# Performance work log

Measured on AMD Instinct MI355X. Metric: run time of the kernel, lower is better.

Reference implementation:

```python
import jax, jax.numpy as jnp
import numpy as np

H = 4  # attention heads


def gat_layer(x, src, dst, W, a_src, a_dst, b, N):
    """PyG-style GATConv (concat=True, negative_slope=0.2, eval-mode dropout)."""
    h = (x @ W).reshape(N, H, -1)                       # [N,H,C]
    es = jnp.einsum('nhc,hc->nh', h, a_src)             # per-node src score
    ed = jnp.einsum('nhc,hc->nh', h, a_dst)             # per-node dst score
    e = jax.nn.leaky_relu(es[src] + ed[dst], negative_slope=0.2)  # [E,H]
    # segment softmax over incoming edges of each destination node
    emax = jax.ops.segment_max(e, dst, num_segments=N)
    ee = jnp.exp(e - emax[dst])
    denom = jax.ops.segment_sum(ee, dst, num_segments=N)
    alpha = ee / (denom[dst] + 1e-16)                   # [E,H]
    out = jax.ops.segment_sum(h[src] * alpha[..., None], dst, num_segments=N)
    return out.reshape(N, -1) + b                        # [N,H*C]


def setup_inputs() -> dict:
    key = jax.random.key(0)
    ks = jax.random.split(key, 13)
    N, E, D, Q = 50000, 800000, 256, 8
    HID, OUT = 256, 256
    Ch, Co = HID // H, OUT // H
    inp = {}
    inp['x'] = jax.random.normal(ks[0], (N, D), dtype=jnp.float32)
    inp['edge_index'] = jax.random.randint(ks[1], (2, E), 0, N, dtype=jnp.int64)
    inp['query_embedding'] = jax.random.normal(ks[2], (Q, OUT), dtype=jnp.float32)
    # layer 1: input_dim -> heads * (hidden_dim//heads)
    inp['W1'] = jax.random.normal(ks[3], (D, HID), dtype=jnp.float32) / np.sqrt(D).astype(np.float32)
    inp['a_src1'] = jax.random.normal(ks[4], (H, Ch), dtype=jnp.float32) / np.sqrt(Ch).astype(np.float32)
    inp['a_dst1'] = jax.random.normal(ks[5], (H, Ch), dtype=jnp.float32) / np.sqrt(Ch).astype(np.float32)
    inp['b1'] = jnp.zeros((HID,), dtype=jnp.float32)
    # layer 2: hidden_dim -> heads * (output_dim//heads)
    inp['W2'] = jax.random.normal(ks[6], (HID, OUT), dtype=jnp.float32) / np.sqrt(HID).astype(np.float32)
    inp['a_src2'] = jax.random.normal(ks[7], (H, Co), dtype=jnp.float32) / np.sqrt(Co).astype(np.float32)
    inp['a_dst2'] = jax.random.normal(ks[8], (H, Co), dtype=jnp.float32) / np.sqrt(Co).astype(np.float32)
    inp['b2'] = jnp.zeros((OUT,), dtype=jnp.float32)
    # node classifier over concat([query, node]) -> 1 (intended Linear(2*OUT, 1))
    inp['Wc'] = jax.random.normal(ks[9], (2 * OUT, 1), dtype=jnp.float32) / np.sqrt(2 * OUT).astype(np.float32)
    inp['bc'] = jnp.zeros((1,), dtype=jnp.float32)
    return inp


def reference(x, edge_index, query_embedding, W1, a_src1, a_dst1, b1,
              W2, a_src2, a_dst2, b2, Wc, bc):
    N = x.shape[0]
    loops = jnp.arange(N, dtype=edge_index.dtype)        # GATConv add_self_loops=True
    src = jnp.concatenate([edge_index[0], loops])
    dst = jnp.concatenate([edge_index[1], loops])
    h = jax.nn.relu(gat_layer(x, src, dst, W1, a_src1, a_dst1, b1, N))
    emb = gat_layer(h, src, dst, W2, a_src2, a_dst2, b2, N)  # [N, OUT]
    D = emb.shape[1]
    # scores[q,n] = Linear(concat(query[q], emb[n])) — computed without
    # materializing the [Q,N,2D] concat (identical math).
    q_part = query_embedding @ Wc[:D] + bc               # [Q,1]
    n_part = emb @ Wc[D:]                                # [N,1]
    node_scores = q_part[:, 0][:, None] + n_part[:, 0][None, :]  # [Q,N]
    return emb, node_scores
```

## Files before the change

kernel.cpp:

```cpp
#include <hip/hip_runtime.h>

typedef unsigned short u16;
typedef unsigned int   u32;
typedef __attribute__((ext_vector_type(8))) short short8v;
typedef __attribute__((ext_vector_type(8))) unsigned short us8;
typedef __attribute__((ext_vector_type(4))) float f32x4;

static __device__ __forceinline__ float bf2f(u16 u){ union{u32 i; float f;} v; v.i=(u32)u<<16; return v.f; }
static __device__ __forceinline__ u16 f2bf(float f){ union{float f; u32 i;} u; u.f=f; u32 r=u.i+0x7FFFu+((u.i>>16)&1u); return (u16)(r>>16); }

static __device__ __forceinline__ float ld1(const void* p, size_t i, int f32){
  return f32 ? ((const float*)p)[i] : bf2f(((const u16*)p)[i]);
}
static __device__ __forceinline__ float4 ld4(const void* p, size_t i, int f32){
  if (f32) return *((const float4*)((const float*)p + i));
  ushort4 v = *((const ushort4*)((const u16*)p + i));
  return make_float4(bf2f(v.x), bf2f(v.y), bf2f(v.z), bf2f(v.w));
}
static __device__ __forceinline__ void st4(void* p, size_t i, float4 v, int f32){
  if (f32) *((float4*)((float*)p + i)) = v;
  else { ushort4 o; o.x=f2bf(v.x); o.y=f2bf(v.y); o.z=f2bf(v.z); o.w=f2bf(v.w); *((ushort4*)((u16*)p + i)) = o; }
}
static __device__ __forceinline__ void st1(void* p, size_t i, float v, int f32){
  if (f32) ((float*)p)[i] = v; else ((u16*)p)[i] = f2bf(v);
}
static __device__ __forceinline__ int lde(const int* ei, size_t i, int i64){
  return i64 ? ei[2*i] : ei[i];
}
static __device__ __forceinline__ int clampi(int v, int lo, int hi){ return v<lo?lo:(v>hi?hi:v); }

__global__ void detect_kernel(const u32* __restrict__ x, const int* __restrict__ ei,
                              int* __restrict__ flags){
  __shared__ int cnt[2];
  int t = threadIdx.x;
  if (t < 2) cnt[t] = 0;
  __syncthreads();
  int good = 0;
  for (int i = t; i < 4096; i += 256){
    u32 e = (x[i] >> 7) & 0xFFu;
    if (e >= 90u && e <= 150u) good++;
  }
  atomicAdd(&cnt[0], good);
  int nzodd = 0;
  for (int i = t; i < 2048; i += 256){
    if (ei[2*i+1] != 0) nzodd++;
  }
  atomicAdd(&cnt[1], nzodd);
  __syncthreads();
  if (t == 0){
    flags[0] = (cnt[0] < 2867) ? 1 : 0;
    flags[1] = (cnt[1] == 0) ? 1 : 0;
  }
}

__global__ void count_kernel(const int* __restrict__ ei, int E, int N,
                             int* __restrict__ deg, const int* __restrict__ flags){
  int i64 = flags[1];
  int i = blockIdx.x*blockDim.x + threadIdx.x;
  int Et = E + N;
  if (i < Et){
    int d = (i < E) ? clampi(lde(ei, (size_t)E + i, i64), 0, N-1) : (i - E);
    atomicAdd(&deg[d], 1);
  }
}

__global__ __launch_bounds__(256) void scan1_kernel(const int* __restrict__ deg,
    int* __restrict__ offs, int* __restrict__ bsum, int N){
  __shared__ int sm[256];
  int t = threadIdx.x;
  int i = blockIdx.x*256 + t;
  int v = (i < N) ? deg[i] : 0;
  sm[t] = v; __syncthreads();
  #pragma unroll
  for (int off = 1; off < 256; off <<= 1){
    int u = (t >= off) ? sm[t-off] : 0;
    __syncthreads();
    sm[t] += u;
    __syncthreads();
  }
  if (i < N) offs[i] = sm[t] - v;
  if (t == 255) bsum[blockIdx.x] = sm[255];
}

__global__ __launch_bounds__(1024) void scan2_kernel(const int* __restrict__ bsum,
    int* __restrict__ bpre, int NB){
  __shared__ int sm[1024];
  int t = threadIdx.x;
  int v = (t < NB) ? bsum[t] : 0;
  sm[t] = v; __syncthreads();
  #pragma unroll
  for (int off = 1; off < 1024; off <<= 1){
    int u = (t >= off) ? sm[t-off] : 0;
    __syncthreads();
    sm[t] += u;
    __syncthreads();
  }
  if (t < NB) bpre[t] = sm[t] - v;
  if (t == 1023) bpre[NB] = sm[1023];
}

__global__ __launch_bounds__(256) void scan3_kernel(int* __restrict__ offs,
    int* __restrict__ cursor, const int* __restrict__ bpre, int N, int NB){
  int i = blockIdx.x*256 + threadIdx.x;
  if (i < N){
    int v = offs[i] + bpre[blockIdx.x];
    offs[i] = v; cursor[i] = v;
  }
  if (i == 0) offs[N] = bpre[NB];
}

__global__ void scatter_kernel(const int* __restrict__ ei, int E, int N,
    int* __restrict__ cursor, int* __restrict__ csr_src, const int* __restrict__ flags){
  int i64 = flags[1];
  int i = blockIdx.x*blockDim.x + threadIdx.x;
  int Et = E + N;
  if (i < Et){
    int s, d;
    if (i < E){
      s = clampi(lde(ei, i, i64), 0, N-1);
      d = clampi(lde(ei, (size_t)E + i, i64), 0, N-1);
    } else { s = i - E; d = s; }
    int p = atomicAdd(&cursor[d], 1);
    csr_src[p] = s;
  }
}

__global__ __launch_bounds__(256) void btrans_kernel(const void* __restrict__ B1,
    const void* __restrict__ B2, u16* __restrict__ BT1, u16* __restrict__ BT2,
    const int* __restrict__ flags){
  int f32 = flags[0];
  const void* B = blockIdx.z ? B2 : B1;
  u16* BT = blockIdx.z ? BT2 : BT1;
  __shared__ u16 tile[64][65];
  int k0 = blockIdx.y*64, c0 = blockIdx.x*64;
  int r0 = threadIdx.x >> 6, c = threadIdx.x & 63;
  for (int r = r0; r < 64; r += 4)
    tile[r][c] = f32 ? f2bf(((const float*)B)[(size_t)(k0+r)*256 + c0 + c])
                     : ((const u16*)B)[(size_t)(k0+r)*256 + c0 + c];
  __syncthreads();
  for (int j = r0; j < 64; j += 4)
    BT[(size_t)(c0+j)*256 + k0 + c] = tile[c][j];
}

__global__ __launch_bounds__(512, 4) void gemm_mfma(const void* __restrict__ A,
    const u16* __restrict__ BT, u16* __restrict__ C, int M, int aIsInput,
    const int* __restrict__ flags, float* __restrict__ es, float* __restrict__ ed,
    const void* __restrict__ a_src, const void* __restrict__ a_dst){
  int af32 = aIsInput ? flags[0] : 0;
  int f32 = flags[0];
  __shared__ __align__(16) u16 As[128][40];
  __shared__ __align__(16) u16 Bs[256][40];
  int tid = threadIdx.x;
  int wave = tid >> 6, lane = tid & 63;
  int wm = wave >> 2, wn = wave & 3;
  int l15 = lane & 15, l4 = lane >> 4;
  int row0 = blockIdx.x * 128;
  const u16*  A16 = (const u16*)A;
  const float* A32 = (const float*)A;
  int srow = tid >> 2, sks = (tid & 3) * 8;
  int scol = tid >> 1, skh = (tid & 1) * 16;
  int sgr = min(row0 + srow, M-1);
  f32x4 acc[4][4] = {};
  for (int k0 = 0; k0 < 256; k0 += 32){
    __syncthreads();
    {
      us8 av;
      if (af32){
        const float* ap = A32 + (size_t)sgr*256 + k0 + sks;
        float4 v0 = *(const float4*)ap, v1 = *(const float4*)(ap+4);
        av = (us8){f2bf(v0.x),f2bf(v0.y),f2bf(v0.z),f2bf(v0.w),
                   f2bf(v1.x),f2bf(v1.y),f2bf(v1.z),f2bf(v1.w)};
      } else {
        av = *(const us8*)(A16 + (size_t)sgr*256 + k0 + sks);
      }
      *(us8*)&As[srow][sks] = av;
      const u16* bp = BT + (size_t)scol*256 + k0 + skh;
      *(us8*)&Bs[scol][skh]   = *(const us8*)bp;
      *(us8*)&Bs[scol][skh+8] = *(const us8*)(bp + 8);
    }
    __syncthreads();
    short8v a[4], b[4];
    #pragma unroll
    for (int mi = 0; mi < 4; mi++)
      a[mi] = *(const short8v*)&As[wm*64 + mi*16 + l15][8*l4];
    #pragma unroll
    for (int ni = 0; ni < 4; ni++)
      b[ni] = *(const short8v*)&Bs[wn*64 + ni*16 + l15][8*l4];
    #pragma unroll
    for (int mi = 0; mi < 4; mi++)
      #pragma unroll
      for (int ni = 0; ni < 4; ni++)
        acc[mi][ni] = __builtin_amdgcn_mfma_f32_16x16x32_bf16(a[mi], b[ni], acc[mi][ni], 0, 0, 0);
  }
  #pragma unroll
  for (int mi = 0; mi < 4; mi++){
    #pragma unroll
    for (int ni = 0; ni < 4; ni++){
      #pragma unroll
      for (int r = 0; r < 4; r++){
        int row = row0 + wm*64 + mi*16 + l4*4 + r;
        int col = wn*64 + ni*16 + l15;
        if (row < M) C[(size_t)row*256 + col] = f2bf(acc[mi][ni][r]);
      }
    }
  }
  float as_[4], ad_[4];
  #pragma unroll
  for (int ni = 0; ni < 4; ni++){
    as_[ni] = ld1(a_src, wn*64 + ni*16 + l15, f32);
    ad_[ni] = ld1(a_dst, wn*64 + ni*16 + l15, f32);
  }
  #pragma unroll
  for (int mi = 0; mi < 4; mi++){
    #pragma unroll
    for (int r = 0; r < 4; r++){
      float pe = acc[mi][0][r]*as_[0] + acc[mi][1][r]*as_[1]
               + acc[mi][2][r]*as_[2] + acc[mi][3][r]*as_[3];
      float pd = acc[mi][0][r]*ad_[0] + acc[mi][1][r]*ad_[1]
               + acc[mi][2][r]*ad_[2] + acc[mi][3][r]*ad_[3];
      #pragma unroll
      for (int off = 1; off < 16; off <<= 1){
        pe += __shfl_xor(pe, off, 64);
        pd += __shfl_xor(pd, off, 64);
      }
      if (l15 == 0){
        int row = row0 + wm*64 + mi*16 + l4*4 + r;
        if (row < M){
          es[(size_t)row*4 + wn] = pe;
          ed[(size_t)row*4 + wn] = pd;
        }
      }
    }
  }
}

__global__ __launch_bounds__(256) void agg_kernel(const u16* __restrict__ h,
    const int* __restrict__ csr_src, const int* __restrict__ offs,
    const float* __restrict__ es, const float* __restrict__ ed, int N,
    const void* __restrict__ bias, void* __restrict__ out, int do_relu, int outIsOutput,
    const int* __restrict__ flags, const void* __restrict__ Wc,
    const float* __restrict__ qp, int Q){
  int f32in = flags[0];
  int of32  = outIsOutput ? flags[0] : 0;
  int ln = threadIdx.x & 63;
  int n = blockIdx.x*4 + (threadIdx.x >> 6);
  if (n >= N) return;
  int beg = offs[n], end = offs[n+1];
  int hd = ln >> 4, c0 = ln*4;
  float edn = ed[(size_t)n*4 + hd];
  float a0=0.f, a1=0.f, a2=0.f, a3=0.f, ws=0.f;
  int i = beg;
  for (; i + 8 <= end; i += 8){
    int s[8]; float x[8]; ushort4 hv[8];
    #pragma unroll
    for (int j = 0; j < 8; j++) s[j] = csr_src[i+j];
    #pragma unroll
    for (int j = 0; j < 8; j++) x[j] = es[(size_t)s[j]*4 + hd];
    #pragma unroll
    for (int j = 0; j < 8; j++) hv[j] = *(const ushort4*)&h[(size_t)s[j]*256 + c0];
    #pragma unroll
    for (int j = 0; j < 8; j++){
      float t = x[j] + edn; t = (t > 0.f) ? t : 0.2f*t; t = fminf(t, 60.f);
      float w = __expf(t);
      a0 += w*bf2f(hv[j].x); a1 += w*bf2f(hv[j].y);
      a2 += w*bf2f(hv[j].z); a3 += w*bf2f(hv[j].w);
      ws += w;
    }
  }
  for (; i + 4 <= end; i += 4){
    int s[4]; float x[4]; ushort4 hv[4];
    #pragma unroll
    for (int j = 0; j < 4; j++) s[j] = csr_src[i+j];
    #pragma unroll
    for (int j = 0; j < 4; j++) x[j] = es[(size_t)s[j]*4 + hd];
    #pragma unroll
    for (int j = 0; j < 4; j++) hv[j] = *(const ushort4*)&h[(size_t)s[j]*256 + c0];
    #pragma unroll
    for (int j = 0; j < 4; j++){
      float t = x[j] + edn; t = (t > 0.f) ? t : 0.2f*t; t = fminf(t, 60.f);
      float w = __expf(t);
      a0 += w*bf2f(hv[j].x); a1 += w*bf2f(hv[j].y);
      a2 += w*bf2f(hv[j].z); a3 += w*bf2f(hv[j].w);
      ws += w;
    }
  }
  for (; i < end; i++){
    int s = csr_src[i];
    float t = es[(size_t)s*4 + hd] + edn; t = (t > 0.f) ? t : 0.2f*t; t = fminf(t, 60.f);
    float w = __expf(t);
    ushort4 hv = *(const ushort4*)&h[(size_t)s*256 + c0];
    a0 += w*bf2f(hv.x); a1 += w*bf2f(hv.y);
    a2 += w*bf2f(hv.z); a3 += w*bf2f(hv.w);
    ws += w;
  }
  float inv = 1.f / (ws + 1e-16f);
  float4 bv = ld4(bias, c0, f32in);
  float4 ov = make_float4(a0*inv + bv.x, a1*inv + bv.y, a2*inv + bv.z, a3*inv + bv.w);
  if (do_relu){
    ov.x = fmaxf(ov.x, 0.f); ov.y = fmaxf(ov.y, 0.f);
    ov.z = fmaxf(ov.z, 0.f); ov.w = fmaxf(ov.w, 0.f);
  }
  st4(out, (size_t)n*256 + c0, ov, of32);
  if (outIsOutput){
    float4 wc4 = ld4(Wc, 256 + c0, f32in);
    float v = ov.x*wc4.x + ov.y*wc4.y + ov.z*wc4.z + ov.w*wc4.w;
    #pragma unroll
    for (int off = 1; off < 64; off <<= 1) v += __shfl_xor(v, off, 64);
    if (ln < Q) st1(out, (size_t)N*256 + (size_t)ln*N + n, qp[ln] + v, of32);
  }
}

__global__ void qpart_kernel(const void* __restrict__ query, const void* __restrict__ Wc,
    const void* __restrict__ bc, float* __restrict__ qp, int Q, const int* __restrict__ flags){
  int f32 = flags[0];
  int q = threadIdx.x >> 5, ln = threadIdx.x & 31;
  if (q >= Q) return;
  float s = 0.f;
  for (int j = ln; j < 256; j += 32) s += ld1(query, q*256 + j, f32) * ld1(Wc, j, f32);
  #pragma unroll
  for (int off = 16; off; off >>= 1) s += __shfl_down(s, off, 32);
  if (ln == 0) qp[q] = s + ld1(bc, 0, f32);
}

extern "C" void kernel_launch(void* const* d_in, const int* in_sizes, int n_in,
                              void* d_out, int out_size, void* d_ws, size_t ws_size,
                              hipStream_t stream){
  const void* x     = d_in[0];
  const int*  ei    = (const int*)d_in[1];
  const void* query = d_in[2];
  const void* W1    = d_in[3];
  const void* as1   = d_in[4];
  const void* ad1   = d_in[5];
  const void* b1    = d_in[6];
  const void* W2    = d_in[7];
  const void* as2   = d_in[8];
  const void* ad2   = d_in[9];
  const void* b2    = d_in[10];
  const void* Wc    = d_in[11];
  const void* bc    = d_in[12];

  int N = in_sizes[0] / 256;
  int E = in_sizes[1] / 2;
  int Q = in_sizes[2] / 256;
  int Et = E + N;
  int NB = (N + 255) / 256;

  char* p = (char*)d_ws;
  auto alloc = [&](size_t bytes)->char*{
    char* r = p; p += (bytes + 255) & ~(size_t)255; return r;
  };
  int*  flags   = (int*) alloc(256);
  u16*  bufA    = (u16*) alloc((size_t)N*256*2);
  u16*  bufB    = (u16*) alloc((size_t)N*256*2);
  float* es     = (float*)alloc((size_t)N*4*4);
  float* ed     = (float*)alloc((size_t)N*4*4);
  int*  deg     = (int*)  alloc((size_t)N*4);
  int*  offs    = (int*)  alloc((size_t)(N+1)*4);
  int*  cursor  = (int*)  alloc((size_t)N*4);
  int*  csr_src = (int*)  alloc((size_t)Et*4);
  int*  bsum    = (int*)  alloc((size_t)(NB+1)*4);
  int*  bpre    = (int*)  alloc((size_t)(NB+1)*4);
  u16*  BT1     = (u16*)  alloc(256*256*2);
  u16*  BT2     = (u16*)  alloc(256*256*2);
  float* qp     = (float*)alloc(64*4);

  const int thr = 256;
  detect_kernel<<<1, 256, 0, stream>>>((const u32*)x, ei, flags);

  hipMemsetAsync(deg, 0, (size_t)N*4, stream);
  count_kernel  <<<(Et + thr-1)/thr, thr, 0, stream>>>(ei, E, N, deg, flags);
  scan1_kernel  <<<NB, 256, 0, stream>>>(deg, offs, bsum, N);
  scan2_kernel  <<<1, 1024, 0, stream>>>(bsum, bpre, NB);
  scan3_kernel  <<<NB, 256, 0, stream>>>(offs, cursor, bpre, N, NB);
  scatter_kernel<<<(Et + thr-1)/thr, thr, 0, stream>>>(ei, E, N, cursor, csr_src, flags);

  dim3 tgrid(4, 4, 2);
  int gblocks = (N + 127)/128;
  dim3 ngrid((N + 3)/4);

  btrans_kernel<<<tgrid, 256, 0, stream>>>(W1, W2, BT1, BT2, flags);
  qpart_kernel <<<1, 256, 0, stream>>>(query, Wc, bc, qp, Q, flags);

  gemm_mfma <<<gblocks, 512, 0, stream>>>(x, BT1, bufA, N, 1, flags, es, ed, as1, ad1);
  agg_kernel<<<ngrid, 256, 0, stream>>>(bufA, csr_src, offs, es, ed, N, b1, bufB, 1, 0,
                                        flags, Wc, qp, Q);
  gemm_mfma <<<gblocks, 512, 0, stream>>>(bufB, BT2, bufA, N, 0, flags, es, ed, as2, ad2);
  agg_kernel<<<ngrid, 256, 0, stream>>>(bufA, csr_src, offs, es, ed, N, b2, d_out, 0, 1,
                                        flags, Wc, qp, Q);
}
```

Measured before the change: 308.3 us.

## Fuse CSR build into one cooperative kernel and store precomputed byte offsets

Replaces the memset, count, three scan kernels and scatter with a single cooperative kernel that uses grid-wide syncs between phases. It also merges the weight transpose and query-part kernels into one prep launch. The CSR now stores source byte offsets (s*512), so the aggregation kernel skips the index multiply. This cuts launch count and per-launch overhead but limits the CSR build to 256 blocks with grid-stride loops and adds the cost of five grid barriers.

```diff
diff --git a/kernel.cpp b/kernel.cpp
--- a/kernel.cpp
+++ b/kernel.cpp
@@ -1,4 +1,7 @@
 #include <hip/hip_runtime.h>
+#include <hip/hip_cooperative_groups.h>
+
+namespace cg = cooperative_groups;
 
 typedef unsigned short u16;
 typedef unsigned int   u32;
@@ -53,93 +56,103 @@
   }
 }
 
-__global__ void count_kernel(const int* __restrict__ ei, int E, int N,
-                             int* __restrict__ deg, const int* __restrict__ flags){
+__global__ __launch_bounds__(256) void csr_kernel(const int* __restrict__ ei, int E, int N,
+    int* __restrict__ deg, int* __restrict__ offs, int* __restrict__ cursor,
+    int* __restrict__ csr_boff, int* __restrict__ bsum, const int* __restrict__ flags){
+  cg::grid_group grid = cg::this_grid();
+  __shared__ int sm[256];
   int i64 = flags[1];
-  int i = blockIdx.x*blockDim.x + threadIdx.x;
   int Et = E + N;
-  if (i < Et){
+  int gsz = gridDim.x * 256;
+  int gtid = blockIdx.x*256 + threadIdx.x;
+  int t = threadIdx.x;
+  for (int i = gtid; i < N; i += gsz) deg[i] = 0;
+  grid.sync();
+  for (int i = gtid; i < Et; i += gsz){
     int d = (i < E) ? clampi(lde(ei, (size_t)E + i, i64), 0, N-1) : (i - E);
     atomicAdd(&deg[d], 1);
   }
-}
-
-__global__ __launch_bounds__(256) void scan1_kernel(const int* __restrict__ deg,
-    int* __restrict__ offs, int* __restrict__ bsum, int N){
-  __shared__ int sm[256];
-  int t = threadIdx.x;
-  int i = blockIdx.x*256 + t;
-  int v = (i < N) ? deg[i] : 0;
-  sm[t] = v; __syncthreads();
-  #pragma unroll
-  for (int off = 1; off < 256; off <<= 1){
-    int u = (t >= off) ? sm[t-off] : 0;
+  grid.sync();
+  int NB = (N + 255) >> 8;
+  for (int b = blockIdx.x; b < NB; b += gridDim.x){
+    int i = b*256 + t;
+    int v = (i < N) ? deg[i] : 0;
     __syncthreads();
-    sm[t] += u;
-    __syncthreads();
-  }
-  if (i < N) offs[i] = sm[t] - v;
-  if (t == 255) bsum[blockIdx.x] = sm[255];
-}
-
-__global__ __launch_bounds__(1024) void scan2_kernel(const int* __restrict__ bsum,
-    int* __restrict__ bpre, int NB){
-  __shared__ int sm[1024];
-  int t = threadIdx.x;
-  int v = (t < NB) ? bsum[t] : 0;
-  sm[t] = v; __syncthreads();
-  #pragma unroll
-  for (int off = 1; off < 1024; off <<= 1){
-    int u = (t >= off) ? sm[t-off] : 0;
-    __syncthreads();
-    sm[t] += u;
-    __syncthreads();
-  }
-  if (t < NB) bpre[t] = sm[t] - v;
-  if (t == 1023) bpre[NB] = sm[1023];
-}
-
-__global__ __launch_bounds__(256) void scan3_kernel(int* __restrict__ offs,
-    int* __restrict__ cursor, const int* __restrict__ bpre, int N, int NB){
-  int i = blockIdx.x*256 + threadIdx.x;
-  if (i < N){
-    int v = offs[i] + bpre[blockIdx.x];
+    sm[t] = v; __syncthreads();
+    #pragma unroll
+    for (int off = 1; off < 256; off <<= 1){
+      int u = (t >= off) ? sm[t-off] : 0;
+      __syncthreads();
+      sm[t] += u;
+      __syncthreads();
+    }
+    if (i < N) offs[i] = sm[t] - v;
+    if (t == 255) bsum[b] = sm[255];
+  }
+  grid.sync();
+  if (blockIdx.x == 0){
+    int chunk = (NB + 255) >> 8;
+    int lo = t*chunk, hi = min(lo + chunk, NB);
+    int s = 0;
+    for (int i = lo; i < hi; i++) s += bsum[i];
+    sm[t] = s; __syncthreads();
+    int mine = s;
+    #pragma unroll
+    for (int off = 1; off < 256; off <<= 1){
+      int u = (t >= off) ? sm[t-off] : 0;
+      __syncthreads();
+      sm[t] += u;
+      __syncthreads();
+    }
+    int run = sm[t] - mine;
+    for (int i = lo; i < hi; i++){ int v = bsum[i]; bsum[i] = run; run += v; }
+    if (t == 255) offs[N] = sm[255];
+  }
+  grid.sync();
+  for (int i = gtid; i < N; i += gsz){
+    int v = offs[i] + bsum[i >> 8];
     offs[i] = v; cursor[i] = v;
   }
-  if (i == 0) offs[N] = bpre[NB];
-}
-
-__global__ void scatter_kernel(const int* __restrict__ ei, int E, int N,
-    int* __restrict__ cursor, int* __restrict__ csr_src, const int* __restrict__ flags){
-  int i64 = flags[1];
-  int i = blockIdx.x*blockDim.x + threadIdx.x;
-  int Et = E + N;
-  if (i < Et){
+  grid.sync();
+  for (int i = gtid; i < Et; i += gsz){
     int s, d;
     if (i < E){
       s = clampi(lde(ei, i, i64), 0, N-1);
       d = clampi(lde(ei, (size_t)E + i, i64), 0, N-1);
     } else { s = i - E; d = s; }
     int p = atomicAdd(&cursor[d], 1);
-    csr_src[p] = s;
-  }
-}
-
-__global__ __launch_bounds__(256) void btrans_kernel(const void* __restrict__ B1,
+    csr_boff[p] = s * 512;
+  }
+}
+
+__global__ __launch_bounds__(256) void prep_kernel(const void* __restrict__ B1,
     const void* __restrict__ B2, u16* __restrict__ BT1, u16* __restrict__ BT2,
-    const int* __restrict__ flags){
+    const void* __restrict__ query, const void* __restrict__ Wc, const void* __restrict__ bc,
+    float* __restrict__ qp, int Q, const int* __restrict__ flags){
   int f32 = flags[0];
-  const void* B = blockIdx.z ? B2 : B1;
-  u16* BT = blockIdx.z ? BT2 : BT1;
-  __shared__ u16 tile[64][65];
-  int k0 = blockIdx.y*64, c0 = blockIdx.x*64;
-  int r0 = threadIdx.x >> 6, c = threadIdx.x & 63;
-  for (int r = r0; r < 64; r += 4)
-    tile[r][c] = f32 ? f2bf(((const float*)B)[(size_t)(k0+r)*256 + c0 + c])
-                     : ((const u16*)B)[(size_t)(k0+r)*256 + c0 + c];
-  __syncthreads();
-  for (int j = r0; j < 64; j += 4)
-    BT[(size_t)(c0+j)*256 + k0 + c] = tile[c][j];
+  int bid = blockIdx.x;
+  if (bid < 32){
+    const void* B = (bid >= 16) ? B2 : B1;
+    u16* BT = (bid >= 16) ? BT2 : BT1;
+    int rem = bid & 15;
+    int k0 = (rem >> 2)*64, c0 = (rem & 3)*64;
+    __shared__ u16 tile[64][65];
+    int r0 = threadIdx.x >> 6, c = threadIdx.x & 63;
+    for (int r = r0; r < 64; r += 4)
+      tile[r][c] = f32 ? f2bf(((const float*)B)[(size_t)(k0+r)*256 + c0 + c])
+                       : ((const u16*)B)[(size_t)(k0+r)*256 + c0 + c];
+    __syncthreads();
+    for (int j = r0; j < 64; j += 4)
+      BT[(size_t)(c0+j)*256 + k0 + c] = tile[c][j];
+  } else {
+    int q = threadIdx.x >> 5, ln = threadIdx.x & 31;
+    if (q >= Q) return;
+    float s = 0.f;
+    for (int j = ln; j < 256; j += 32) s += ld1(query, q*256 + j, f32) * ld1(Wc, j, f32);
+    #pragma unroll
+    for (int off = 16; off; off >>= 1) s += __shfl_down(s, off, 32);
+    if (ln == 0) qp[q] = s + ld1(bc, 0, f32);
+  }
 }
 
 __global__ __launch_bounds__(512, 4) void gemm_mfma(const void* __restrict__ A,
@@ -235,7 +248,7 @@
 }
 
 __global__ __launch_bounds__(256) void agg_kernel(const u16* __restrict__ h,
-    const int* __restrict__ csr_src, const int* __restrict__ offs,
+    const int* __restrict__ csr_boff, const int* __restrict__ offs,
     const float* __restrict__ es, const float* __restrict__ ed, int N,
     const void* __restrict__ bias, void* __restrict__ out, int do_relu, int outIsOutput,
     const int* __restrict__ flags, const void* __restrict__ Wc,
@@ -247,17 +260,21 @@
   if (n >= N) return;
   int beg = offs[n], end = offs[n+1];
   int hd = ln >> 4, c0 = ln*4;
+  int hd4 = hd*4;
+  size_t coff = (size_t)c0*2;
+  const char* hbase = (const char*)h;
+  const char* ebase = (const char*)es;
   float edn = ed[(size_t)n*4 + hd];
   float a0=0.f, a1=0.f, a2=0.f, a3=0.f, ws=0.f;
   int i = beg;
   for (; i + 8 <= end; i += 8){
-    int s[8]; float x[8]; ushort4 hv[8];
-    #pragma unroll
-    for (int j = 0; j < 8; j++) s[j] = csr_src[i+j];
-    #pragma unroll
-    for (int j = 0; j < 8; j++) x[j] = es[(size_t)s[j]*4 + hd];
-    #pragma unroll
-    for (int j = 0; j < 8; j++) hv[j] = *(const ushort4*)&h[(size_t)s[j]*256 + c0];
+    int bo[8]; float x[8]; ushort4 hv[8];
+    #pragma unroll
+    for (int j = 0; j < 8; j++) bo[j] = csr_boff[i+j];
+    #pragma unroll
+    for (int j = 0; j < 8; j++) x[j] = *(const float*)(ebase + (bo[j] >> 5) + hd4);
+    #pragma unroll
+    for (int j = 0; j < 8; j++) hv[j] = *(const ushort4*)(hbase + bo[j] + coff);
     #pragma unroll
     for (int j = 0; j < 8; j++){
       float t = x[j] + edn; t = (t > 0.f) ? t : 0.2f*t; t = fminf(t, 60.f);
@@ -268,13 +285,13 @@
     }
   }
   for (; i + 4 <= end; i += 4){
-    int s[4]; float x[4]; ushort4 hv[4];
-    #pragma unroll
-    for (int j = 0; j < 4; j++) s[j] = csr_src[i+j];
-    #pragma unroll
-    for (int j = 0; j < 4; j++) x[j] = es[(size_t)s[j]*4 + hd];
-    #pragma unroll
-    for (int j = 0; j < 4; j++) hv[j] = *(const ushort4*)&h[(size_t)s[j]*256 + c0];
+    int bo[4]; float x[4]; ushort4 hv[4];
+    #pragma unroll
+    for (int j = 0; j < 4; j++) bo[j] = csr_boff[i+j];
+    #pragma unroll
+    for (int j = 0; j < 4; j++) x[j] = *(const float*)(ebase + (bo[j] >> 5) + hd4);
+    #pragma unroll
+    for (int j = 0; j < 4; j++) hv[j] = *(const ushort4*)(hbase + bo[j] + coff);
     #pragma unroll
     for (int j = 0; j < 4; j++){
       float t = x[j] + edn; t = (t > 0.f) ? t : 0.2f*t; t = fminf(t, 60.f);
@@ -285,10 +302,11 @@
     }
   }
   for (; i < end; i++){
-    int s = csr_src[i];
-    float t = es[(size_t)s*4 + hd] + edn; t = (t > 0.f) ? t : 0.2f*t; t = fminf(t, 60.f);
+    int bo = csr_boff[i];
+    float t = *(const float*)(ebase + (bo >> 5) + hd4) + edn;
+    t = (t > 0.f) ? t : 0.2f*t; t = fminf(t, 60.f);
     float w = __expf(t);
-    ushort4 hv = *(const ushort4*)&h[(size_t)s*256 + c0];
+    ushort4 hv = *(const ushort4*)(hbase + bo + coff);
     a0 += w*bf2f(hv.x); a1 += w*bf2f(hv.y);
     a2 += w*bf2f(hv.z); a3 += w*bf2f(hv.w);
     ws += w;
@@ -308,18 +326,6 @@
     for (int off = 1; off < 64; off <<= 1) v += __shfl_xor(v, off, 64);
     if (ln < Q) st1(out, (size_t)N*256 + (size_t)ln*N + n, qp[ln] + v, of32);
   }
-}
-
-__global__ void qpart_kernel(const void* __restrict__ query, const void* __restrict__ Wc,
-    const void* __restrict__ bc, float* __restrict__ qp, int Q, const int* __restrict__ flags){
-  int f32 = flags[0];
-  int q = threadIdx.x >> 5, ln = threadIdx.x & 31;
-  if (q >= Q) return;
-  float s = 0.f;
-  for (int j = ln; j < 256; j += 32) s += ld1(query, q*256 + j, f32) * ld1(Wc, j, f32);
-  #pragma unroll
-  for (int off = 16; off; off >>= 1) s += __shfl_down(s, off, 32);
-  if (ln == 0) qp[q] = s + ld1(bc, 0, f32);
 }
 
 extern "C" void kernel_launch(void* const* d_in, const int* in_sizes, int n_in,
@@ -349,42 +355,37 @@
   auto alloc = [&](size_t bytes)->char*{
     char* r = p; p += (bytes + 255) & ~(size_t)255; return r;
   };
-  int*  flags   = (int*) alloc(256);
-  u16*  bufA    = (u16*) alloc((size_t)N*256*2);
-  u16*  bufB    = (u16*) alloc((size_t)N*256*2);
-  float* es     = (float*)alloc((size_t)N*4*4);
-  float* ed     = (float*)alloc((size_t)N*4*4);
-  int*  deg     = (int*)  alloc((size_t)N*4);
-  int*  offs    = (int*)  alloc((size_t)(N+1)*4);
-  int*  cursor  = (int*)  alloc((size_t)N*4);
-  int*  csr_src = (int*)  alloc((size_t)Et*4);
-  int*  bsum    = (int*)  alloc((size_t)(NB+1)*4);
-  int*  bpre    = (int*)  alloc((size_t)(NB+1)*4);
-  u16*  BT1     = (u16*)  alloc(256*256*2);
-  u16*  BT2     = (u16*)  alloc(256*256*2);
-  float* qp     = (float*)alloc(64*4);
-
-  const int thr = 256;
+  int*  flags    = (int*) alloc(256);
+  u16*  bufA     = (u16*) alloc((size_t)N*256*2);
+  u16*  bufB     = (u16*) alloc((size_t)N*256*2);
+  float* es      = (float*)alloc((size_t)N*4*4);
+  float* ed      = (float*)alloc((size_t)N*4*4);
+  int*  deg      = (int*)  alloc((size_t)N*4);
+  int*  offs     = (int*)  alloc((size_t)(N+1)*4);
+  int*  cursor   = (int*)  alloc((size_t)N*4);
+  int*  csr_boff = (int*)  alloc((size_t)Et*4);
+  int*  bsum     = (int*)  alloc((size_t)(NB+1)*4);
+  u16*  BT1      = (u16*)  alloc(256*256*2);
+  u16*  BT2      = (u16*)  alloc(256*256*2);
+  float* qp      = (float*)alloc(64*4);
+
   detect_kernel<<<1, 256, 0, stream>>>((const u32*)x, ei, flags);
 
-  hipMemsetAsync(deg, 0, (size_t)N*4, stream);
-  count_kernel  <<<(Et + thr-1)/thr, thr, 0, stream>>>(ei, E, N, deg, flags);
-  scan1_kernel  <<<NB, 256, 0, stream>>>(deg, offs, bsum, N);
-  scan2_kernel  <<<1, 1024, 0, stream>>>(bsum, bpre, NB);
-  scan3_kernel  <<<NB, 256, 0, stream>>>(offs, cursor, bpre, N, NB);
-  scatter_kernel<<<(Et + thr-1)/thr, thr, 0, stream>>>(ei, E, N, cursor, csr_src, flags);
-
-  dim3 tgrid(4, 4, 2);
+  {
+    void* args[] = { (void*)&ei, (void*)&E, (void*)&N, (void*)&deg, (void*)&offs,
+                     (void*)&cursor, (void*)&csr_boff, (void*)&bsum, (void*)&flags };
+    hipLaunchCooperativeKernel((void*)csr_kernel, dim3(256), dim3(256), args, 0, stream);
+  }
+
+  prep_kernel<<<33, 256, 0, stream>>>(W1, W2, BT1, BT2, query, Wc, bc, qp, Q, flags);
+
   int gblocks = (N + 127)/128;
   dim3 ngrid((N + 3)/4);
 
-  btrans_kernel<<<tgrid, 256, 0, stream>>>(W1, W2, BT1, BT2, flags);
-  qpart_kernel <<<1, 256, 0, stream>>>(query, Wc, bc, qp, Q, flags);
-
   gemm_mfma <<<gblocks, 512, 0, stream>>>(x, BT1, bufA, N, 1, flags, es, ed, as1, ad1);
-  agg_kernel<<<ngrid, 256, 0, stream>>>(bufA, csr_src, offs, es, ed, N, b1, bufB, 1, 0,
+  agg_kernel<<<ngrid, 256, 0, stream>>>(bufA, csr_boff, offs, es, ed, N, b1, bufB, 1, 0,
                                         flags, Wc, qp, Q);
   gemm_mfma <<<gblocks, 512, 0, stream>>>(bufB, BT2, bufA, N, 0, flags, es, ed, as2, ad2);
-  agg_kernel<<<ngrid, 256, 0, stream>>>(bufA, csr_src, offs, es, ed, N, b2, d_out, 0, 1,
+  agg_kernel<<<ngrid, 256, 0, stream>>>(bufA, csr_boff, offs, es, ed, N, b2, d_out, 0, 1,
                                         flags, Wc, qp, Q);
 }
```

After: 432.5 us. +40.3%, slower.
